# Kernel optimization log

Hardware: AMD Instinct MI355X
Metric: run time of the kernel (lower is better)

Reference implementation:

```python
import jax, jax.numpy as jnp
import numpy as np

EPS = 1e-12
W_MAX = 0.8
ALPHA_MAX = 1.5
EXP_CLIP = 20.0
UNARY_TEMP = 1.5
T = 10
ETA = 0.2
ALPHA_SCALE = 1.0

N_NODES = 50000
N_PAIRS = 400000          # undirected pairs; E = 2*N_PAIRS directed edges
IN_DIM = 256
HID = 128
C = 10
EDGE_HID = 64


def setup_inputs() -> dict:
    key = jax.random.key(0)
    ks = jax.random.split(key, 12)
    x = jax.random.normal(ks[0], (N_NODES, IN_DIM), dtype=jnp.float32)
    # symmetric edge list: each undirected pair appears in both directions,
    # rev[e] gives the index of the reversed edge
    src = jax.random.randint(ks[1], (N_PAIRS,), 0, N_NODES, dtype=jnp.int32)
    dst = jax.random.randint(ks[2], (N_PAIRS,), 0, N_NODES, dtype=jnp.int32)
    edge_index = jnp.stack([jnp.concatenate([src, dst]),
                            jnp.concatenate([dst, src])])  # [2, E]
    rev = jnp.concatenate([jnp.arange(N_PAIRS, 2 * N_PAIRS, dtype=jnp.int32),
                           jnp.arange(0, N_PAIRS, dtype=jnp.int32)])
    def lin(k, fan_in, fan_out):
        s = 1.0 / np.sqrt(fan_in)
        return jax.random.uniform(k, (fan_in, fan_out), jnp.float32, -s, s)
    enc_w1 = lin(ks[3], IN_DIM, HID); enc_b1 = jnp.zeros((HID,), jnp.float32)
    enc_w2 = lin(ks[4], HID, C);      enc_b2 = jnp.zeros((C,), jnp.float32)
    em_in = 2 * HID + 2
    em_w1 = lin(ks[5], em_in, EDGE_HID); em_b1 = jnp.zeros((EDGE_HID,), jnp.float32)
    em_w2 = lin(ks[6], EDGE_HID, 1);     em_b2 = jnp.zeros((1,), jnp.float32)
    # xavier_uniform for R_raw
    bound = np.sqrt(6.0 / (C + C))
    R_raw = jax.random.uniform(ks[7], (C, C), jnp.float32, -bound, bound)
    R_scale_log = jnp.asarray(0.0, jnp.float32)
    msg_logit = jnp.asarray(-1.0, jnp.float32)
    return {"x": x, "edge_index": edge_index, "rev": rev,
            "enc_w1": enc_w1, "enc_b1": enc_b1, "enc_w2": enc_w2, "enc_b2": enc_b2,
            "em_w1": em_w1, "em_b1": em_b1, "em_w2": em_w2, "em_b2": em_b2,
            "R_raw": R_raw, "R_scale_log": R_scale_log, "msg_logit": msg_logit}


def reference(x, edge_index, rev, enc_w1, enc_b1, enc_w2, enc_b2,
              em_w1, em_b1, em_w2, em_b2, R_raw, R_scale_log, msg_logit):
    num_nodes = x.shape[0]
    src, dst = edge_index[0], edge_index[1]

    # --- UnaryEncoder (mlp, eval mode: no dropout) ---
    h = jax.nn.relu(x @ enc_w1 + enc_b1)                       # [N, H]
    logits = h @ enc_w2 + enc_b2                               # [N, C]
    log_phi = jax.nn.log_softmax(logits / UNARY_TEMP, axis=-1)

    # --- edge structural features ---
    deg = jax.ops.segment_sum(jnp.ones_like(src, jnp.float32), src,
                              num_segments=num_nodes)           # bincount(src)
    logdeg = jnp.log(deg + 1.0)
    a, b = logdeg[src], logdeg[dst]
    struct = jnp.stack([a + b, jnp.abs(a - b)], axis=-1)        # [E, 2]

    # --- pairwise kernel ---
    hs, hd = h[src], h[dst]
    edge_in = jnp.concatenate([hs * hd, jnp.abs(hs - hd), struct], axis=-1)
    w_raw = (jax.nn.relu(edge_in @ em_w1 + em_b1) @ em_w2 + em_b2)[:, 0]
    w = W_MAX * jax.nn.sigmoid(w_raw)
    w = 0.5 * (w + w[rev])                                      # symmetrize
    R = (jax.nn.softplus(R_scale_log) + 1e-6) * jnp.tanh(0.5 * (R_raw + R_raw.T))
    K = jnp.exp(jnp.clip(w[:, None, None] * R[None], -EXP_CLIP, EXP_CLIP))  # [E,C,C]

    # --- BP ---
    deg_c = jnp.maximum(deg, 1.0)
    edge_norm = (deg_c[src] * deg_c[dst]) ** -0.5               # [E]
    alpha = ALPHA_MAX * jax.nn.sigmoid(msg_logit) * ALPHA_SCALE
    lp_src = log_phi[src]
    m0 = jax.nn.softmax(lp_src, axis=-1)                        # init_unary=True

    def step(m, _):
        f = jnp.einsum('ec,ecd->ed', m, K)
        f = jnp.nan_to_num(f, nan=1.0, posinf=1.0, neginf=1.0)
        log_f = jnp.log(jnp.maximum(f, EPS)) * edge_norm[:, None]
        sum_in = jax.ops.segment_sum(log_f, dst, num_segments=num_nodes)
        excl = sum_in[src] - log_f[rev]
        m_new = jax.nn.softmax(lp_src + alpha * excl, axis=-1)
        m = (1.0 - ETA) * m + ETA * m_new
        m = jnp.maximum(m, EPS)
        m = m / jnp.sum(m, axis=-1, keepdims=True)
        return m, None

    m, _ = jax.lax.scan(step, m0, None, length=T)

    # --- beliefs ---
    f = jnp.einsum('ec,ecd->ed', m, K)
    f = jnp.nan_to_num(f, nan=1.0, posinf=1.0, neginf=1.0)
    log_f = jnp.log(jnp.maximum(f, EPS)) * edge_norm[:, None]
    sum_in = jax.ops.segment_sum(log_f, dst, num_segments=num_nodes)
    beliefs = jax.nn.softmax(log_phi + alpha * sum_in, axis=-1)  # [N, C]
    return beliefs
```

## Files before the change

### kernel.cpp

```cpp
#include <hip/hip_runtime.h>
#include <hip/hip_fp16.h>

#define NN 50000
#define NP 400000
#define NEDGE 800000
#define IND 256
#define HD 128
#define NC 10
#define TBP 10
#define SCAN_NB 196

typedef _Float16 f16;
typedef _Float16 f16x2 __attribute__((ext_vector_type(2)));
typedef _Float16 f16x4 __attribute__((ext_vector_type(4)));
typedef _Float16 f16x8 __attribute__((ext_vector_type(8)));
typedef unsigned short u16x8 __attribute__((ext_vector_type(8)));
typedef float f32x4 __attribute__((ext_vector_type(4)));

static constexpr size_t OFF_R      = 0;
static constexpr size_t OFF_H      = 512;
static constexpr size_t OFF_OFFS   = 512;
static constexpr size_t OFF_CUR    = 512 + 200016;
static constexpr size_t OFF_POS    = 512 + 400032;
static constexpr size_t OFF_BSUM   = 512 + 3600032;
static constexpr size_t OFF_BBASE  = 512 + 3601056;
static constexpr size_t OFF_LOGPHI = 12800512;
static constexpr size_t OFF_DEG    = 14800512;
static constexpr size_t OFF_LOGDEG = 15000512;
static constexpr size_t OFF_RSQ    = 15200512;
static constexpr size_t OFF_WPAIR  = 15400512;
static constexpr size_t OFF_EN     = 17000512;
static constexpr size_t OFF_M      = 18600512;
static constexpr size_t OFF_L      = 50600512;
static constexpr size_t OFF_SUMIN  = 82600512;
static constexpr size_t OFF_W1T    = 84600512;
static constexpr size_t OFF_W1TE   = 84633280;

__global__ __launch_bounds__(256) void k_setup(const float* __restrict__ Rraw,
    const float* __restrict__ rsl, const float* __restrict__ ml,
    const float* __restrict__ mw1, const float* __restrict__ ew1,
    float* __restrict__ Rbuf, f16* __restrict__ w1t, f16* __restrict__ w1te) {
  int tid = threadIdx.x;
  if (tid < 100) {
    int c = tid / 10, d = tid % 10;
    float scale = log1pf(expf(rsl[0])) + 1e-6f;
    Rbuf[tid] = scale * tanhf(0.5f * (Rraw[c * 10 + d] + Rraw[d * 10 + c]));
  } else if (tid == 100) {
    Rbuf[100] = 1.5f * (1.f / (1.f + expf(-ml[0])));
  }
  for (int idx = tid; idx < 64 * 256; idx += 256) {
    int j = idx >> 8, k = idx & 255;
    w1t[idx] = (f16)mw1[k * 64 + j];
  }
  for (int idx = tid; idx < 128 * 256; idx += 256) {
    int j = idx >> 8, k = idx & 255;
    w1te[idx] = (f16)ew1[k * HD + j];
  }
}

__global__ __launch_bounds__(256) void k_deg(const int* __restrict__ ei, float* __restrict__ deg) {
  int e = blockIdx.x * 256 + threadIdx.x;
  if (e < NEDGE) atomicAdd(&deg[ei[e]], 1.f);
}

__global__ __launch_bounds__(256) void k_nodepost(const float* __restrict__ deg,
    float* __restrict__ logdeg, float* __restrict__ rsq) {
  int i = blockIdx.x * 256 + threadIdx.x;
  if (i >= NN) return;
  float d = deg[i];
  logdeg[i] = __logf(d + 1.f);
  rsq[i] = rsqrtf(fmaxf(d, 1.f));
}

__global__ __launch_bounds__(256) void k_scan1(const float* __restrict__ deg,
    int* __restrict__ bsum) {
  int idx = blockIdx.x * 256 + threadIdx.x;
  int v = (idx < NN) ? (int)deg[idx] : 0;
#pragma unroll
  for (int o = 32; o; o >>= 1) v += __shfl_down(v, o);
  __shared__ int wsum[4];
  if ((threadIdx.x & 63) == 0) wsum[threadIdx.x >> 6] = v;
  __syncthreads();
  if (threadIdx.x == 0) bsum[blockIdx.x] = wsum[0] + wsum[1] + wsum[2] + wsum[3];
}

__global__ __launch_bounds__(256) void k_scan2(const int* __restrict__ bsum,
    int* __restrict__ bbase) {
  __shared__ int s[256];
  int t = threadIdx.x;
  int orig = (t < SCAN_NB) ? bsum[t] : 0;
  s[t] = orig;
  __syncthreads();
  for (int d = 1; d < 256; d <<= 1) {
    int v = (t >= d) ? s[t - d] : 0;
    __syncthreads();
    s[t] += v;
    __syncthreads();
  }
  bbase[t] = s[t] - orig;
}

__global__ __launch_bounds__(256) void k_scan3(const float* __restrict__ deg,
    const int* __restrict__ bbase, int* __restrict__ off, int* __restrict__ cursor) {
  __shared__ int s[256];
  int t = threadIdx.x;
  int idx = blockIdx.x * 256 + t;
  int d = (idx < NN) ? (int)deg[idx] : 0;
  s[t] = d;
  __syncthreads();
  for (int k = 1; k < 256; k <<= 1) {
    int v = (t >= k) ? s[t - k] : 0;
    __syncthreads();
    s[t] += v;
    __syncthreads();
  }
  int base = bbase[blockIdx.x];
  int excl = base + s[t] - d;
  if (idx < NN) {
    off[idx] = excl;
    cursor[idx] = excl;
  }
  if (idx == NN - 1) off[NN] = excl + d;
}

__global__ __launch_bounds__(256) void k_fill(const int* __restrict__ ei,
    int* __restrict__ cursor, int* __restrict__ pos) {
  int e = blockIdx.x * 256 + threadIdx.x;
  if (e >= NEDGE) return;
  int d = ei[NEDGE + e];
  pos[e] = atomicAdd(&cursor[d], 1);
}

__global__ __launch_bounds__(256) void k_encoder(const float* __restrict__ x,
    const f16* __restrict__ w1te, const float* __restrict__ b1, f16* __restrict__ h) {
  __shared__ f16 As[64 * 264];
  const int tid = threadIdx.x;
  const int wid = tid >> 6;
  const int lane = tid & 63;
  const int l15 = lane & 15;
  const int lhi = lane >> 4;
  const int nb = blockIdx.x * 64;
#pragma unroll
  for (int i = 0; i < 16; i++) {
    int fidx = tid + 256 * i;
    int row = fidx >> 6;
    int q = fidx & 63;
    f32x4 v = {0.f, 0.f, 0.f, 0.f};
    if (nb + row < NN) v = *(const f32x4*)(x + (size_t)(nb + row) * IND + q * 4);
    f16x4 o;
#pragma unroll
    for (int j = 0; j < 4; j++) o[j] = (f16)v[j];
    *(f16x4*)(&As[row * 264 + q * 4]) = o;
  }
  __syncthreads();
  f16x8 bfr[8][2];
#pragma unroll
  for (int ks = 0; ks < 8; ks++)
#pragma unroll
    for (int t = 0; t < 2; t++)
      bfr[ks][t] = *(const f16x8*)(w1te + (size_t)(wid * 32 + t * 16 + l15) * 256 + ks * 32 + lhi * 8);
  float b1v[2] = {b1[wid * 32 + l15], b1[wid * 32 + 16 + l15]};
  f32x4 acc[4][2] = {};
#pragma unroll
  for (int ks = 0; ks < 8; ks++) {
    f16x8 af[4];
#pragma unroll
    for (int rt = 0; rt < 4; rt++)
      af[rt] = *(const f16x8*)(&As[(rt * 16 + l15) * 264 + ks * 32 + lhi * 8]);
#pragma unroll
    for (int rt = 0; rt < 4; rt++)
#pragma unroll
      for (int t = 0; t < 2; t++)
        acc[rt][t] = __builtin_amdgcn_mfma_f32_16x16x32_f16(af[rt], bfr[ks][t], acc[rt][t], 0, 0, 0);
  }
#pragma unroll
  for (int rt = 0; rt < 4; rt++) {
#pragma unroll
    for (int t = 0; t < 2; t++) {
#pragma unroll
      for (int i = 0; i < 4; i++) {
        int row = nb + rt * 16 + lhi * 4 + i;
        if (row < NN)
          h[(size_t)row * HD + wid * 32 + t * 16 + l15] = (f16)fmaxf(acc[rt][t][i] + b1v[t], 0.f);
      }
    }
  }
}

__global__ __launch_bounds__(256) void k_logits(const f16* __restrict__ h,
    const float* __restrict__ w2, const float* __restrict__ b2, float* __restrict__ logphi) {
  __shared__ float hs[16 * HD];
  __shared__ float lg[16 * NC];
  const int tid = threadIdx.x;
  const int nb = blockIdx.x * 16;
  for (int i = tid; i < 16 * HD / 8; i += 256) {
    f16x8 v = *(const f16x8*)(h + (size_t)nb * HD + i * 8);
#pragma unroll
    for (int u = 0; u < 8; u++) hs[i * 8 + u] = (float)v[u];
  }
  __syncthreads();
  if (tid < 160) {
    int n = tid / 10, c = tid % 10;
    float a = b2[c];
    for (int k = 0; k < HD; k++) a += hs[n * HD + k] * w2[k * NC + c];
    lg[n * NC + c] = a * (1.f / 1.5f);
  }
  __syncthreads();
  if (tid < 16) {
    float mx = -1e30f;
#pragma unroll
    for (int c = 0; c < NC; c++) mx = fmaxf(mx, lg[tid * NC + c]);
    float s = 0.f;
#pragma unroll
    for (int c = 0; c < NC; c++) s += __expf(lg[tid * NC + c] - mx);
    float lse = __logf(s) + mx;
#pragma unroll
    for (int c = 0; c < NC; c++)
      logphi[(size_t)(nb + tid) * NC + c] = lg[tid * NC + c] - lse;
  }
}

__global__ __launch_bounds__(256) void k_edge_mlp(const f16* __restrict__ h,
    const int* __restrict__ ei, const float* __restrict__ logdeg, const float* __restrict__ rsq,
    const f16* __restrict__ w1t, const float* __restrict__ mw1, const float* __restrict__ mb1,
    const float* __restrict__ mw2, const float* __restrict__ mb2,
    float* __restrict__ w_pair, float* __restrict__ en_pair) {
  __shared__ f16 At[4][16 * 264];
  __shared__ float hidl[4][16 * 64];
  __shared__ float sfeat[4][2][16];
  const int tid = threadIdx.x;
  const int wid = tid >> 6;
  const int lane = tid & 63;
  const int l15 = lane & 15;
  const int lhi = lane >> 4;

  f16x8 bfr[8][4];
#pragma unroll
  for (int ks = 0; ks < 8; ks++)
#pragma unroll
    for (int t = 0; t < 4; t++)
      bfr[ks][t] = *(const f16x8*)(w1t + (size_t)(l15 + 16 * t) * 256 + ks * 32 + lhi * 8);

  float b1v[4], w256v[4], w257v[4];
#pragma unroll
  for (int t = 0; t < 4; t++) {
    b1v[t] = mb1[l15 + 16 * t];
    w256v[t] = mw1[256 * 64 + l15 + 16 * t];
    w257v[t] = mw1[257 * 64 + l15 + 16 * t];
  }
  float w2r[16];
#pragma unroll
  for (int jj = 0; jj < 16; jj++) w2r[jj] = mw2[lhi * 16 + jj];
  const float b2s = mb2[0];

  const int ntiles = NP / 64;
  for (int tile = blockIdx.x; tile < ntiles; tile += gridDim.x) {
    const int pbase = tile * 64 + wid * 16;
#pragma unroll
    for (int rr = 0; rr < 4; rr++) {
      int r = rr * 4 + lhi;
      int p = pbase + r;
      int s = ei[p], d = ei[NEDGE + p];
      f16x8 hv = *(const f16x8*)(h + (size_t)s * HD + l15 * 8);
      f16x8 gv = *(const f16x8*)(h + (size_t)d * HD + l15 * 8);
      f16x8 pv = hv * gv;
      f16x8 qv = hv - gv;
      u16x8 qb = *(u16x8*)&qv;
#pragma unroll
      for (int u = 0; u < 8; u++) qb[u] &= 0x7FFF;
      qv = *(f16x8*)&qb;
      *(f16x8*)(&At[wid][r * 264 + l15 * 8]) = pv;
      *(f16x8*)(&At[wid][r * 264 + 128 + l15 * 8]) = qv;
    }
    if (lane < 16) {
      int p = pbase + lane;
      int s = ei[p], d = ei[NEDGE + p];
      float a = logdeg[s], b = logdeg[d];
      sfeat[wid][0][lane] = a + b;
      sfeat[wid][1][lane] = fabsf(a - b);
      en_pair[p] = rsq[s] * rsq[d];
    }
    __syncthreads();
    f32x4 acc[4] = {{0.f, 0.f, 0.f, 0.f}, {0.f, 0.f, 0.f, 0.f},
                    {0.f, 0.f, 0.f, 0.f}, {0.f, 0.f, 0.f, 0.f}};
#pragma unroll
    for (int ks = 0; ks < 8; ks++) {
      f16x8 af = *(const f16x8*)(&At[wid][l15 * 264 + ks * 32 + lhi * 8]);
#pragma unroll
      for (int t = 0; t < 4; t++)
        acc[t] = __builtin_amdgcn_mfma_f32_16x16x32_f16(af, bfr[ks][t], acc[t], 0, 0, 0);
    }
#pragma unroll
    for (int t = 0; t < 4; t++) {
#pragma unroll
      for (int i = 0; i < 4; i++) {
        int r = lhi * 4 + i;
        float v = acc[t][i] + sfeat[wid][0][r] * w256v[t] + sfeat[wid][1][r] * w257v[t] + b1v[t];
        hidl[wid][r * 64 + l15 + 16 * t] = fmaxf(v, 0.f);
      }
    }
    __syncthreads();
    {
      float sacc = 0.f;
#pragma unroll
      for (int jj = 0; jj < 16; jj++) sacc += hidl[wid][l15 * 64 + lhi * 16 + jj] * w2r[jj];
      sacc += __shfl_xor(sacc, 16);
      sacc += __shfl_xor(sacc, 32);
      if (lane < 16) {
        float wr = sacc + b2s;
        w_pair[pbase + lane] = 0.8f / (1.f + __expf(-wr));
      }
    }
    __syncthreads();
  }
}

__global__ __launch_bounds__(256) void k_m0(const int* __restrict__ ei,
    const float* __restrict__ logphi, f16* __restrict__ m) {
  int e = blockIdx.x * 256 + threadIdx.x;
  if (e >= NEDGE) return;
  int s = ei[e];
  f16x2* mp = (f16x2*)(m + (size_t)e * 10);
  const float2* lp = (const float2*)(logphi + (size_t)s * 10);
#pragma unroll
  for (int i = 0; i < 5; i++) {
    float2 v = lp[i];
    f16x2 o;
    o[0] = (f16)__expf(v.x);
    o[1] = (f16)__expf(v.y);
    mp[i] = o;
  }
}

__global__ __launch_bounds__(256) void k_bp_f(const f16* __restrict__ m,
    const float* __restrict__ wp, const float* __restrict__ enp,
    const int* __restrict__ pos, const float* __restrict__ Rbuf, f16* __restrict__ L) {
  __shared__ float Rs[100];
  if (threadIdx.x < 100) Rs[threadIdx.x] = Rbuf[threadIdx.x];
  __syncthreads();
  int e = blockIdx.x * 256 + threadIdx.x;
  if (e >= NEDGE) return;
  int p = (e < NP) ? e : e - NP;
  float w = wp[p], en = enp[p];
  float mr[10];
  {
    const f16x2* mp = (const f16x2*)(m + (size_t)e * 10);
#pragma unroll
    for (int i = 0; i < 5; i++) { f16x2 v = mp[i]; mr[2 * i] = (float)v[0]; mr[2 * i + 1] = (float)v[1]; }
  }
  float f[10] = {0, 0, 0, 0, 0, 0, 0, 0, 0, 0};
#pragma unroll
  for (int c = 0; c < NC; c++) {
    float Ecc = __expf(w * Rs[c * NC + c]);
    f[c] += mr[c] * Ecc;
#pragma unroll
    for (int d = c + 1; d < NC; d++) {
      float Ecd = __expf(w * Rs[c * NC + d]);
      f[d] += mr[c] * Ecd;
      f[c] += mr[d] * Ecd;
    }
  }
  f16x2* Lp = (f16x2*)(L + (size_t)pos[e] * 10);
#pragma unroll
  for (int i = 0; i < 5; i++) {
    f16x2 o;
    o[0] = (f16)(__logf(fmaxf(f[2 * i], 1e-12f)) * en);
    o[1] = (f16)(__logf(fmaxf(f[2 * i + 1], 1e-12f)) * en);
    Lp[i] = o;
  }
}

__global__ __launch_bounds__(256) void k_gather(const f16* __restrict__ L,
    const int* __restrict__ off, float* __restrict__ sumin) {
  int wave = (blockIdx.x * 256 + threadIdx.x) >> 6;
  int lane = threadIdx.x & 63;
  int nl = lane / 10;
  int c = lane % 10;
  int n = wave * 6 + nl;
  if (nl >= 6 || n >= NN) return;
  int o0 = off[n], o1 = off[n + 1];
  float acc = 0.f;
  for (int k = o0; k < o1; k++) acc += (float)L[(size_t)k * 10 + c];
  sumin[(size_t)n * 10 + c] = acc;
}

__global__ __launch_bounds__(256) void k_bp_fused(f16* __restrict__ m,
    f16* __restrict__ L, const float* __restrict__ sumin,
    const float* __restrict__ logphi, const int* __restrict__ ei,
    const int* __restrict__ pos,
    const float* __restrict__ wp, const float* __restrict__ enp,
    const float* __restrict__ Rbuf) {
  __shared__ float Rs[104];
  if (threadIdx.x < 101) Rs[threadIdx.x] = Rbuf[threadIdx.x];
  __syncthreads();
  int p = blockIdx.x * 256 + threadIdx.x;
  if (p >= NP) return;
  const float alpha = Rs[100];
  const int s = ei[p], d = ei[NEDGE + p];
  const float w = wp[p], en = enp[p];
  const int pe = pos[p], pr = pos[p + NP];

  float Le[10], Lr[10];
  {
    const f16x2* a = (const f16x2*)(L + (size_t)pe * 10);
    const f16x2* b = (const f16x2*)(L + (size_t)pr * 10);
#pragma unroll
    for (int i = 0; i < 5; i++) {
      f16x2 u = a[i], v = b[i];
      Le[2 * i] = (float)u[0]; Le[2 * i + 1] = (float)u[1];
      Lr[2 * i] = (float)v[0]; Lr[2 * i + 1] = (float)v[1];
    }
  }
  float te[10], tr[10];
  float mxe = -1e30f, mxr = -1e30f;
  {
    const float2* sis = (const float2*)(sumin + (size_t)s * 10);
    const float2* sid = (const float2*)(sumin + (size_t)d * 10);
    const float2* lps = (const float2*)(logphi + (size_t)s * 10);
    const float2* lpd = (const float2*)(logphi + (size_t)d * 10);
#pragma unroll
    for (int i = 0; i < 5; i++) {
      float2 ss = sis[i], sd = sid[i], ps = lps[i], pd = lpd[i];
      float e0 = ps.x + alpha * (ss.x - Lr[2 * i]);
      float e1 = ps.y + alpha * (ss.y - Lr[2 * i + 1]);
      float r0 = pd.x + alpha * (sd.x - Le[2 * i]);
      float r1 = pd.y + alpha * (sd.y - Le[2 * i + 1]);
      te[2 * i] = e0; te[2 * i + 1] = e1;
      tr[2 * i] = r0; tr[2 * i + 1] = r1;
      mxe = fmaxf(mxe, fmaxf(e0, e1));
      mxr = fmaxf(mxr, fmaxf(r0, r1));
    }
  }
  float se = 0.f, sr = 0.f;
#pragma unroll
  for (int c = 0; c < NC; c++) {
    float ve = __expf(te[c] - mxe);
    float vr = __expf(tr[c] - mxr);
    te[c] = ve; tr[c] = vr;
    se += ve; sr += vr;
  }
  const float ie = 0.2f / se, ir = 0.2f / sr;
  float me[10], mr[10];
  float nse = 0.f, nsr = 0.f;
  {
    f16x2* mpe = (f16x2*)(m + (size_t)p * 10);
    f16x2* mpr = (f16x2*)(m + (size_t)(p + NP) * 10);
#pragma unroll
    for (int i = 0; i < 5; i++) {
      f16x2 u = mpe[i], v = mpr[i];
      float a0 = fmaxf(0.8f * (float)u[0] + te[2 * i] * ie, 1e-12f);
      float a1 = fmaxf(0.8f * (float)u[1] + te[2 * i + 1] * ie, 1e-12f);
      float b0 = fmaxf(0.8f * (float)v[0] + tr[2 * i] * ir, 1e-12f);
      float b1 = fmaxf(0.8f * (float)v[1] + tr[2 * i + 1] * ir, 1e-12f);
      me[2 * i] = a0; me[2 * i + 1] = a1;
      mr[2 * i] = b0; mr[2 * i + 1] = b1;
      nse += a0 + a1; nsr += b0 + b1;
    }
    const float qe = 1.f / nse, qr = 1.f / nsr;
#pragma unroll
    for (int i = 0; i < 5; i++) {
      me[2 * i] *= qe; me[2 * i + 1] *= qe;
      mr[2 * i] *= qr; mr[2 * i + 1] *= qr;
      f16x2 u, v;
      u[0] = (f16)me[2 * i]; u[1] = (f16)me[2 * i + 1];
      v[0] = (f16)mr[2 * i]; v[1] = (f16)mr[2 * i + 1];
      mpe[i] = u; mpr[i] = v;
    }
  }
  float fe[10] = {0, 0, 0, 0, 0, 0, 0, 0, 0, 0};
  float fr[10] = {0, 0, 0, 0, 0, 0, 0, 0, 0, 0};
#pragma unroll
  for (int c = 0; c < NC; c++) {
    float Ecc = __expf(w * Rs[c * NC + c]);
    fe[c] += me[c] * Ecc;
    fr[c] += mr[c] * Ecc;
#pragma unroll
    for (int dd = c + 1; dd < NC; dd++) {
      float E = __expf(w * Rs[c * NC + dd]);
      fe[dd] += me[c] * E; fe[c] += me[dd] * E;
      fr[dd] += mr[c] * E; fr[c] += mr[dd] * E;
    }
  }
  {
    f16x2* Lpe = (f16x2*)(L + (size_t)pe * 10);
    f16x2* Lpr = (f16x2*)(L + (size_t)pr * 10);
#pragma unroll
    for (int i = 0; i < 5; i++) {
      f16x2 u, v;
      u[0] = (f16)(__logf(fmaxf(fe[2 * i], 1e-12f)) * en);
      u[1] = (f16)(__logf(fmaxf(fe[2 * i + 1], 1e-12f)) * en);
      v[0] = (f16)(__logf(fmaxf(fr[2 * i], 1e-12f)) * en);
      v[1] = (f16)(__logf(fmaxf(fr[2 * i + 1], 1e-12f)) * en);
      Lpe[i] = u; Lpr[i] = v;
    }
  }
}

__global__ __launch_bounds__(256) void k_beliefs(const float* __restrict__ logphi,
    const float* __restrict__ sum_in, const float* __restrict__ Rbuf, float* __restrict__ out) {
  int n = blockIdx.x * 256 + threadIdx.x;
  if (n >= NN) return;
  float alpha = Rbuf[100];
  float t[NC];
  float mx = -1e30f;
#pragma unroll
  for (int c = 0; c < NC; c++) {
    float v = logphi[n * NC + c] + alpha * sum_in[n * NC + c];
    t[c] = v;
    mx = fmaxf(mx, v);
  }
  float ssum = 0.f;
#pragma unroll
  for (int c = 0; c < NC; c++) { float ev = __expf(t[c] - mx); t[c] = ev; ssum += ev; }
  float inv = 1.f / ssum;
#pragma unroll
  for (int c = 0; c < NC; c++) out[(size_t)n * NC + c] = t[c] * inv;
}

extern "C" void kernel_launch(void* const* d_in, const int* in_sizes, int n_in,
                              void* d_out, int out_size, void* d_ws, size_t ws_size,
                              hipStream_t stream) {
  const float* x    = (const float*)d_in[0];
  const int*   ei   = (const int*)d_in[1];
  const float* ew1  = (const float*)d_in[3];
  const float* eb1  = (const float*)d_in[4];
  const float* ew2  = (const float*)d_in[5];
  const float* eb2  = (const float*)d_in[6];
  const float* mw1  = (const float*)d_in[7];
  const float* mb1  = (const float*)d_in[8];
  const float* mw2  = (const float*)d_in[9];
  const float* mb2  = (const float*)d_in[10];
  const float* Rraw = (const float*)d_in[11];
  const float* rsl  = (const float*)d_in[12];
  const float* ml   = (const float*)d_in[13];
  float* out = (float*)d_out;

  char* ws = (char*)d_ws;
  float* Rbuf   = (float*)(ws + OFF_R);
  f16*   h      = (f16*)(ws + OFF_H);
  int*   offs   = (int*)(ws + OFF_OFFS);
  int*   cursor = (int*)(ws + OFF_CUR);
  int*   pos    = (int*)(ws + OFF_POS);
  int*   bsum   = (int*)(ws + OFF_BSUM);
  int*   bbase  = (int*)(ws + OFF_BBASE);
  float* logphi = (float*)(ws + OFF_LOGPHI);
  float* deg    = (float*)(ws + OFF_DEG);
  float* logdeg = (float*)(ws + OFF_LOGDEG);
  float* rsq    = (float*)(ws + OFF_RSQ);
  float* wpair  = (float*)(ws + OFF_WPAIR);
  float* enp    = (float*)(ws + OFF_EN);
  f16*   m      = (f16*)(ws + OFF_M);
  f16*   L      = (f16*)(ws + OFF_L);
  float* sumin  = (float*)(ws + OFF_SUMIN);
  f16*   w1t    = (f16*)(ws + OFF_W1T);
  f16*   w1te   = (f16*)(ws + OFF_W1TE);

  k_setup<<<1, 256, 0, stream>>>(Rraw, rsl, ml, mw1, ew1, Rbuf, w1t, w1te);
  hipMemsetAsync(deg, 0, NN * sizeof(float), stream);
  k_deg<<<NEDGE / 256, 256, 0, stream>>>(ei, deg);
  k_nodepost<<<(NN + 255) / 256, 256, 0, stream>>>(deg, logdeg, rsq);
  k_encoder<<<(NN + 63) / 64, 256, 0, stream>>>(x, w1te, eb1, h);
  k_logits<<<NN / 16, 256, 0, stream>>>(h, ew2, eb2, logphi);
  k_edge_mlp<<<512, 256, 0, stream>>>(h, ei, logdeg, rsq, w1t, mw1, mb1, mw2, mb2, wpair, enp);
  k_scan1<<<SCAN_NB, 256, 0, stream>>>(deg, bsum);
  k_scan2<<<1, 256, 0, stream>>>(bsum, bbase);
  k_scan3<<<SCAN_NB, 256, 0, stream>>>(deg, bbase, offs, cursor);
  k_fill<<<NEDGE / 256, 256, 0, stream>>>(ei, cursor, pos);
  k_m0<<<NEDGE / 256, 256, 0, stream>>>(ei, logphi, m);
  k_bp_f<<<NEDGE / 256, 256, 0, stream>>>(m, wpair, enp, pos, Rbuf, L);

  const int gblocks = (NN + 23) / 24;
  const int fblocks = (NP + 255) / 256;
  for (int it = 0; it < TBP; it++) {
    k_gather<<<gblocks, 256, 0, stream>>>(L, offs, sumin);
    k_bp_fused<<<fblocks, 256, 0, stream>>>(m, L, sumin, logphi, ei, pos, wpair, enp, Rbuf);
  }
  k_gather<<<gblocks, 256, 0, stream>>>(L, offs, sumin);
  k_beliefs<<<(NN + 255) / 256, 256, 0, stream>>>(logphi, sumin, Rbuf, out);
}
```

Before: 1.076 ms.

## Store L in edge order and gather through a CSR edge index list

L was stored in destination-sorted order, so the segment-sum gather read it contiguously while the edge kernels wrote and read it at scattered positions. Now L is kept in edge order, which makes the edge-update kernels' L accesses coalesced. The gather instead goes through an explicit CSR list of edge ids, so it adds one index load per edge and reads L at scattered rows. The change trades scattered accesses in the edge kernels for indirect scattered reads in the gather.

```diff
diff --git a/kernel.cpp b/kernel.cpp
--- a/kernel.cpp
+++ b/kernel.cpp
@@ -21,7 +21,7 @@
 static constexpr size_t OFF_H      = 512;
 static constexpr size_t OFF_OFFS   = 512;
 static constexpr size_t OFF_CUR    = 512 + 200016;
-static constexpr size_t OFF_POS    = 512 + 400032;
+static constexpr size_t OFF_CSR    = 512 + 400032;
 static constexpr size_t OFF_BSUM   = 512 + 3600032;
 static constexpr size_t OFF_BBASE  = 512 + 3601056;
 static constexpr size_t OFF_LOGPHI = 12800512;
@@ -124,11 +124,12 @@
 }
 
 __global__ __launch_bounds__(256) void k_fill(const int* __restrict__ ei,
-    int* __restrict__ cursor, int* __restrict__ pos) {
+    int* __restrict__ cursor, int* __restrict__ csr) {
   int e = blockIdx.x * 256 + threadIdx.x;
   if (e >= NEDGE) return;
   int d = ei[NEDGE + e];
-  pos[e] = atomicAdd(&cursor[d], 1);
+  int slot = atomicAdd(&cursor[d], 1);
+  csr[slot] = e;
 }
 
 __global__ __launch_bounds__(256) void k_encoder(const float* __restrict__ x,
@@ -334,7 +335,7 @@
 
 __global__ __launch_bounds__(256) void k_bp_f(const f16* __restrict__ m,
     const float* __restrict__ wp, const float* __restrict__ enp,
-    const int* __restrict__ pos, const float* __restrict__ Rbuf, f16* __restrict__ L) {
+    const float* __restrict__ Rbuf, f16* __restrict__ L) {
   __shared__ float Rs[100];
   if (threadIdx.x < 100) Rs[threadIdx.x] = Rbuf[threadIdx.x];
   __syncthreads();
@@ -360,7 +361,7 @@
       f[c] += mr[d] * Ecd;
     }
   }
-  f16x2* Lp = (f16x2*)(L + (size_t)pos[e] * 10);
+  f16x2* Lp = (f16x2*)(L + (size_t)e * 10);
 #pragma unroll
   for (int i = 0; i < 5; i++) {
     f16x2 o;
@@ -371,7 +372,7 @@
 }
 
 __global__ __launch_bounds__(256) void k_gather(const f16* __restrict__ L,
-    const int* __restrict__ off, float* __restrict__ sumin) {
+    const int* __restrict__ csr, const int* __restrict__ off, float* __restrict__ sumin) {
   int wave = (blockIdx.x * 256 + threadIdx.x) >> 6;
   int lane = threadIdx.x & 63;
   int nl = lane / 10;
@@ -380,14 +381,16 @@
   if (nl >= 6 || n >= NN) return;
   int o0 = off[n], o1 = off[n + 1];
   float acc = 0.f;
-  for (int k = o0; k < o1; k++) acc += (float)L[(size_t)k * 10 + c];
+  for (int k = o0; k < o1; k++) {
+    int e = csr[k];
+    acc += (float)L[(size_t)e * 10 + c];
+  }
   sumin[(size_t)n * 10 + c] = acc;
 }
 
 __global__ __launch_bounds__(256) void k_bp_fused(f16* __restrict__ m,
     f16* __restrict__ L, const float* __restrict__ sumin,
     const float* __restrict__ logphi, const int* __restrict__ ei,
-    const int* __restrict__ pos,
     const float* __restrict__ wp, const float* __restrict__ enp,
     const float* __restrict__ Rbuf) {
   __shared__ float Rs[104];
@@ -398,12 +401,11 @@
   const float alpha = Rs[100];
   const int s = ei[p], d = ei[NEDGE + p];
   const float w = wp[p], en = enp[p];
-  const int pe = pos[p], pr = pos[p + NP];
 
   float Le[10], Lr[10];
   {
-    const f16x2* a = (const f16x2*)(L + (size_t)pe * 10);
-    const f16x2* b = (const f16x2*)(L + (size_t)pr * 10);
+    const f16x2* a = (const f16x2*)(L + (size_t)p * 10);
+    const f16x2* b = (const f16x2*)(L + (size_t)(p + NP) * 10);
 #pragma unroll
     for (int i = 0; i < 5; i++) {
       f16x2 u = a[i], v = b[i];
@@ -482,8 +484,8 @@
     }
   }
   {
-    f16x2* Lpe = (f16x2*)(L + (size_t)pe * 10);
-    f16x2* Lpr = (f16x2*)(L + (size_t)pr * 10);
+    f16x2* Lpe = (f16x2*)(L + (size_t)p * 10);
+    f16x2* Lpr = (f16x2*)(L + (size_t)(p + NP) * 10);
 #pragma unroll
     for (int i = 0; i < 5; i++) {
       f16x2 u, v;
@@ -540,7 +542,7 @@
   f16*   h      = (f16*)(ws + OFF_H);
   int*   offs   = (int*)(ws + OFF_OFFS);
   int*   cursor = (int*)(ws + OFF_CUR);
-  int*   pos    = (int*)(ws + OFF_POS);
+  int*   csr    = (int*)(ws + OFF_CSR);
   int*   bsum   = (int*)(ws + OFF_BSUM);
   int*   bbase  = (int*)(ws + OFF_BBASE);
   float* logphi = (float*)(ws + OFF_LOGPHI);
@@ -565,16 +567,16 @@
   k_scan1<<<SCAN_NB, 256, 0, stream>>>(deg, bsum);
   k_scan2<<<1, 256, 0, stream>>>(bsum, bbase);
   k_scan3<<<SCAN_NB, 256, 0, stream>>>(deg, bbase, offs, cursor);
-  k_fill<<<NEDGE / 256, 256, 0, stream>>>(ei, cursor, pos);
+  k_fill<<<NEDGE / 256, 256, 0, stream>>>(ei, cursor, csr);
   k_m0<<<NEDGE / 256, 256, 0, stream>>>(ei, logphi, m);
-  k_bp_f<<<NEDGE / 256, 256, 0, stream>>>(m, wpair, enp, pos, Rbuf, L);
+  k_bp_f<<<NEDGE / 256, 256, 0, stream>>>(m, wpair, enp, Rbuf, L);
 
   const int gblocks = (NN + 23) / 24;
   const int fblocks = (NP + 255) / 256;
   for (int it = 0; it < TBP; it++) {
-    k_gather<<<gblocks, 256, 0, stream>>>(L, offs, sumin);
-    k_bp_fused<<<fblocks, 256, 0, stream>>>(m, L, sumin, logphi, ei, pos, wpair, enp, Rbuf);
-  }
-  k_gather<<<gblocks, 256, 0, stream>>>(L, offs, sumin);
+    k_gather<<<gblocks, 256, 0, stream>>>(L, csr, offs, sumin);
+    k_bp_fused<<<fblocks, 256, 0, stream>>>(m, L, sumin, logphi, ei, wpair, enp, Rbuf);
+  }
+  k_gather<<<gblocks, 256, 0, stream>>>(L, csr, offs, sumin);
   k_beliefs<<<(NN + 255) / 256, 256, 0, stream>>>(logphi, sumin, Rbuf, out);
 }
```

Measured after the change: 990.9 us. 7.9% less time.
